# Optimization experiments

Measured on AMD Instinct MI355X. Metric: run time of the kernel, lower is better.

The kernel has to match this reference:

```python
import jax, jax.numpy as jnp
import numpy as np

U = 128  # GRU units
NIDS = 1000  # shared-state table rows

def hard_sigmoid(x):
    return jnp.clip(0.2 * x + 0.5, 0.0, 1.0)

def setup_inputs() -> dict:
    key = jax.random.key(0)
    ks = jax.random.split(key, 8)
    B, T, F = 4096, 200, 18
    inputs = jax.random.normal(ks[0], (B, T, F), dtype=jnp.float32)
    ids = jax.random.randint(ks[1], (B, T), 0, NIDS)
    inputs = inputs.at[:, :, 0].set(ids.astype(jnp.float32))
    kernel = jax.random.normal(ks[2], (F, 3 * U), dtype=jnp.float32) * 0.15
    recurrent_kernel = jax.random.normal(ks[3], (U, 3 * U), dtype=jnp.float32) * 0.08
    bias = jnp.zeros((3 * U,), dtype=jnp.float32)
    shared0 = jnp.zeros((NIDS, U), dtype=jnp.float32)
    w1 = jax.random.normal(ks[4], (U, 64), dtype=jnp.float32) * 0.1
    b1 = jnp.zeros((64,), dtype=jnp.float32)
    w2 = jax.random.normal(ks[5], (64, 1), dtype=jnp.float32) * 0.1
    b2 = jnp.zeros((1,), dtype=jnp.float32)
    return {"inputs": inputs, "kernel": kernel, "recurrent_kernel": recurrent_kernel,
            "bias": bias, "shared0": shared0, "w1": w1, "b1": b1, "w2": w2, "b2": b2}

def reference(inputs, kernel, recurrent_kernel, bias, shared0, w1, b1, w2, b2):
    # inputs: [B, T, F]; column 0 holds card ids (float-encoded).
    def step(carry, x_t):
        shared = carry  # [NIDS, U]
        ids = x_t[:, 0].astype(jnp.int32)          # [B]
        h = shared[ids]                             # gather [B, U]
        mx = x_t @ kernel + bias                    # [B, 3U]
        mh = h @ recurrent_kernel[:, :2 * U]        # [B, 2U]
        z = hard_sigmoid(mx[:, :U] + mh[:, :U])
        r = hard_sigmoid(mx[:, U:2 * U] + mh[:, U:])
        hh = jnp.tanh(mx[:, 2 * U:] + (r * h) @ recurrent_kernel[:, 2 * U:])
        h_new = z * h + (1.0 - z) * hh
        shared = shared.at[ids].set(h_new)          # scatter update
        return shared, h_new
    xs = jnp.swapaxes(inputs, 0, 1)                 # [T, B, F]
    _, hs = jax.lax.scan(step, shared0, xs)
    h_last = hs[-1]                                 # RNN returns last output [B, U]
    # dropout is identity at inference
    d = jax.nn.relu(h_last @ w1 + b1)
    out = jax.nn.sigmoid(d @ w2 + b2)               # [B, 1]
    return out
```

## Files before the change

kernel.cpp:

```cpp
#include <hip/hip_runtime.h>
#include <math.h>

#define Bz   4096
#define Tz   200
#define Fz   18
#define Uz   128
#define NIDS 1000
#define NCH  4
#define NWG  250

__device__ __forceinline__ float hsig(float x) {
    return fminf(fmaxf(fmaf(x, 0.2f, 0.5f), 0.0f), 1.0f);
}
__device__ __forceinline__ float rlane(float v, int l) {
    return __int_as_float(__builtin_amdgcn_readlane(__float_as_int(v), l));
}

__global__ void k_winner(const float* __restrict__ in, int* __restrict__ win) {
    int idx = blockIdx.x * blockDim.x + threadIdx.x;
    if (idx >= Bz * Tz) return;
    int b = idx / Tz, t = idx - b * Tz;
    int id = (int)in[(size_t)idx * Fz];
    id = min(max(id, 0), NIDS - 1);
    atomicMax(&win[t * NIDS + id], b);
}

template<bool MASK>
__device__ __forceinline__ void gstep(
    int tid, int w, int lane, int l15,
    const float (&wzr)[16][4], const float (&wh)[16][2],
    const float (&wk1)[3][4], const float (&wk2)[3][2],
    int f0, int f1, int f2,
    float breg, float breg2,
    float4* hlds, float4* ubuf, float4* zbuf, float4* p1, float4* p2,
    float xa, float xb, int4 act)
{
    float4 hd4 = hlds[w * 16 + l15];
    float hdj[4] = {hd4.x, hd4.y, hd4.z, hd4.w};
    float az[4][4];
#pragma unroll
    for (int i = 0; i < 4; ++i) { az[i][0]=0.f; az[i][1]=0.f; az[i][2]=0.f; az[i][3]=0.f; }

    int fs[3] = {f0, f1, f2};
#pragma unroll
    for (int ff = 0; ff < 3; ++ff) {
        int fb = fs[ff];
#pragma unroll
        for (int j = 0; j < 4; ++j) {
            float xv = (j < 2) ? rlane(xa, j * 18 + fb) : rlane(xb, (j - 2) * 18 + fb);
#pragma unroll
            for (int i = 0; i < 4; ++i) az[i][j] = fmaf(xv, wk1[ff][i], az[i][j]);
        }
    }
#pragma unroll
    for (int kl = 0; kl < 16; ++kl) {
#pragma unroll
        for (int j = 0; j < 4; ++j) {
            float hv = rlane(hdj[j], kl);
#pragma unroll
            for (int i = 0; i < 4; ++i) az[i][j] = fmaf(hv, wzr[kl][i], az[i][j]);
        }
    }
#pragma unroll
    for (int i = 0; i < 4; ++i)
        p1[w * 256 + lane + 64 * i] = make_float4(az[i][0], az[i][1], az[i][2], az[i][3]);
    __syncthreads();

    if (tid < 256) {
        int c = tid;
        float4 s = p1[c];
#pragma unroll
        for (int ww = 1; ww < 8; ++ww) {
            float4 q = p1[ww * 256 + c];
            s.x += q.x; s.y += q.y; s.z += q.z; s.w += q.w;
        }
        s.x += breg; s.y += breg; s.z += breg; s.w += breg;
        if (c < 128) {
            zbuf[c] = make_float4(hsig(s.x), hsig(s.y), hsig(s.z), hsig(s.w));
        } else {
            int cc = c - 128;
            float4 ho = hlds[cc];
            ubuf[cc] = make_float4(hsig(s.x) * ho.x, hsig(s.y) * ho.y,
                                   hsig(s.z) * ho.z, hsig(s.w) * ho.w);
        }
    }
    __syncthreads();

    float4 ud4 = ubuf[w * 16 + l15];
    float udj[4] = {ud4.x, ud4.y, ud4.z, ud4.w};
    float p[2][4];
#pragma unroll
    for (int i = 0; i < 2; ++i) { p[i][0]=0.f; p[i][1]=0.f; p[i][2]=0.f; p[i][3]=0.f; }
#pragma unroll
    for (int ff = 0; ff < 3; ++ff) {
        int fb = fs[ff];
#pragma unroll
        for (int j = 0; j < 4; ++j) {
            float xv = (j < 2) ? rlane(xa, j * 18 + fb) : rlane(xb, (j - 2) * 18 + fb);
#pragma unroll
            for (int i = 0; i < 2; ++i) p[i][j] = fmaf(xv, wk2[ff][i], p[i][j]);
        }
    }
#pragma unroll
    for (int kl = 0; kl < 16; ++kl) {
#pragma unroll
        for (int j = 0; j < 4; ++j) {
            float uv = rlane(udj[j], kl);
#pragma unroll
            for (int i = 0; i < 2; ++i) p[i][j] = fmaf(uv, wh[kl][i], p[i][j]);
        }
    }
    p2[w * 128 + lane]      = make_float4(p[0][0], p[0][1], p[0][2], p[0][3]);
    p2[w * 128 + lane + 64] = make_float4(p[1][0], p[1][1], p[1][2], p[1][3]);
    __syncthreads();

    if (tid < 128) {
        int c = tid;
        float4 s = p2[c];
#pragma unroll
        for (int ww = 1; ww < 8; ++ww) {
            float4 q = p2[ww * 128 + c];
            s.x += q.x; s.y += q.y; s.z += q.z; s.w += q.w;
        }
        float hh0 = tanhf(s.x + breg2), hh1 = tanhf(s.y + breg2);
        float hh2 = tanhf(s.z + breg2), hh3 = tanhf(s.w + breg2);
        float4 z = zbuf[c], ho = hlds[c];
        float n0 = fmaf(z.x, ho.x - hh0, hh0);
        float n1 = fmaf(z.y, ho.y - hh1, hh1);
        float n2 = fmaf(z.z, ho.z - hh2, hh2);
        float n3 = fmaf(z.w, ho.w - hh3, hh3);
        if (MASK) {
            if (act.x < 0) n0 = ho.x;
            if (act.y < 0) n1 = ho.y;
            if (act.z < 0) n2 = ho.z;
            if (act.w < 0) n3 = ho.w;
        }
        hlds[c] = make_float4(n0, n1, n2, n3);
    }
    __syncthreads();
}

#define LOAD_WEIGHTS                                                         \
    float wzr[16][4], wh[16][2], wk1[3][4], wk2[3][2];                       \
    _Pragma("unroll")                                                        \
    for (int kl = 0; kl < 16; ++kl) {                                        \
        int row = (w * 16 + kl) * 384;                                       \
        _Pragma("unroll")                                                    \
        for (int i = 0; i < 4; ++i) wzr[kl][i] = rk[row + lane + 64 * i];    \
        _Pragma("unroll")                                                    \
        for (int i = 0; i < 2; ++i) wh[kl][i] = rk[row + 256 + lane + 64*i]; \
    }                                                                        \
    int f0 = 2 * w, f1 = 2 * w + 1, f2 = (w < 2) ? 16 + w : 0;               \
    {                                                                        \
        int r0 = f0 * 384, r1 = f1 * 384, r2 = f2 * 384;                     \
        _Pragma("unroll")                                                    \
        for (int i = 0; i < 4; ++i) {                                        \
            wk1[0][i] = ker[r0 + lane + 64 * i];                             \
            wk1[1][i] = ker[r1 + lane + 64 * i];                             \
            wk1[2][i] = (w < 2) ? ker[r2 + lane + 64 * i] : 0.0f;            \
        }                                                                    \
        _Pragma("unroll")                                                    \
        for (int i = 0; i < 2; ++i) {                                        \
            wk2[0][i] = ker[r0 + 256 + lane + 64 * i];                       \
            wk2[1][i] = ker[r1 + 256 + lane + 64 * i];                       \
            wk2[2][i] = (w < 2) ? ker[r2 + 256 + lane + 64 * i] : 0.0f;      \
        }                                                                    \
    }                                                                        \
    float breg  = (tid < 256) ? bias[tid] : 0.0f;                            \
    float breg2 = (tid < 128) ? bias[256 + tid] : 0.0f;

__global__ __launch_bounds__(512, 2)
void k_scan(const float* __restrict__ in,  const float* __restrict__ ker,
            const float* __restrict__ rk,  const float* __restrict__ bias,
            const float* __restrict__ sh0, const int* __restrict__ win,
            float* __restrict__ sfinal)
{
    const int tid  = threadIdx.x;
    const int bx   = blockIdx.x;
    const int w    = tid >> 6;
    const int lane = tid & 63;
    const int l15  = lane & 15;

    __shared__ __align__(16) float4 hlds[Uz], ubuf[Uz], zbuf[Uz];
    __shared__ __align__(16) float4 p1[8 * 256];
    __shared__ __align__(16) float4 p2[8 * 128];

    LOAD_WEIGHTS

    ((float*)hlds)[tid] = sh0[(bx * 4 + (tid & 3)) * Uz + (tid >> 2)];

    const int4* winp = (const int4*)win;
    int4 wv_cur = winp[bx];
    int4 wv_nxt = winp[NWG + bx];

    auto ldx = [&](int4 wv, int t, int jb) -> float {
        if (lane >= 36) return 0.0f;
        int j = lane / 18, f = lane - j * 18;
        int jj = jb + j;
        int b = (jj == 0) ? wv.x : (jj == 1) ? wv.y : (jj == 2) ? wv.z : wv.w;
        if (b < 0) return 0.0f;
        return in[((size_t)b * Tz + t) * Fz + f];
    };
    float xa = ldx(wv_cur, 0, 0), xb = ldx(wv_cur, 0, 2);
    __syncthreads();

    for (int t = 0; t < Tz - 1; ++t) {
        int tf = (t + 2 < Tz) ? t + 2 : Tz - 1;
        int4  wv_fut = winp[tf * NWG + bx];
        float xaN = ldx(wv_nxt, t + 1, 0);
        float xbN = ldx(wv_nxt, t + 1, 2);

        gstep<true>(tid, w, lane, l15, wzr, wh, wk1, wk2, f0, f1, f2,
                    breg, breg2, hlds, ubuf, zbuf, p1, p2, xa, xb, wv_cur);

        xa = xaN; xb = xbN; wv_cur = wv_nxt; wv_nxt = wv_fut;
    }

    sfinal[bx * 512 + tid] = ((float*)hlds)[tid];
}

__global__ __launch_bounds__(512, 2)
void k_final(const float* __restrict__ in,  const float* __restrict__ ker,
             const float* __restrict__ rk,  const float* __restrict__ bias,
             const float* __restrict__ sfinal,
             const float* __restrict__ w1,  const float* __restrict__ b1,
             const float* __restrict__ w2,  const float* __restrict__ b2,
             float* __restrict__ out)
{
    const int tid  = threadIdx.x;
    const int w    = tid >> 6;
    const int lane = tid & 63;
    const int l15  = lane & 15;

    __shared__ __align__(16) float4 hlds[Uz], ubuf[Uz], zbuf[Uz];
    __shared__ __align__(16) float4 p1[8 * 256];
    __shared__ __align__(16) float4 p2[8 * 128];

    LOAD_WEIGHTS

    for (int it = 0; it < 4; ++it) {
        int bbase = blockIdx.x * 16 + it * 4;
        {
            int j  = tid & 3, c = tid >> 2;
            int id = (int)in[((size_t)(bbase + j) * Tz + (Tz - 1)) * Fz];
            id = min(max(id, 0), NIDS - 1);
            ((float*)hlds)[tid] = sfinal[((id >> 2) * Uz + c) * 4 + (id & 3)];
        }
        float xa = 0.0f, xb = 0.0f;
        if (lane < 36) {
            int j = lane / 18, f = lane - j * 18;
            xa = in[((size_t)(bbase + j)     * Tz + (Tz - 1)) * Fz + f];
            xb = in[((size_t)(bbase + 2 + j) * Tz + (Tz - 1)) * Fz + f];
        }
        __syncthreads();

        gstep<false>(tid, w, lane, l15, wzr, wh, wk1, wk2, f0, f1, f2,
                     breg, breg2, hlds, ubuf, zbuf, p1, p2, xa, xb,
                     make_int4(0, 0, 0, 0));

        if (tid < 256) {
            int j  = tid >> 6, un = tid & 63;
            float dacc = b1[un];
#pragma unroll
            for (int k = 0; k < Uz; ++k)
                dacc = fmaf(((const float*)hlds)[k * 4 + j], w1[k * 64 + un], dacc);
            float v = fmaxf(dacc, 0.0f) * w2[un];
#pragma unroll
            for (int off = 32; off > 0; off >>= 1) v += __shfl_xor(v, off, 64);
            if (un == 0)
                out[bbase + j] = 1.0f / (1.0f + expf(-(v + b2[0])));
        }
        __syncthreads();
    }
}

extern "C" void kernel_launch(void* const* d_in, const int* in_sizes, int n_in,
                              void* d_out, int out_size, void* d_ws, size_t ws_size,
                              hipStream_t stream) {
    const float* in   = (const float*)d_in[0];
    const float* ker  = (const float*)d_in[1];
    const float* rk   = (const float*)d_in[2];
    const float* bias = (const float*)d_in[3];
    const float* sh0  = (const float*)d_in[4];
    const float* w1   = (const float*)d_in[5];
    const float* b1   = (const float*)d_in[6];
    const float* w2   = (const float*)d_in[7];
    const float* b2   = (const float*)d_in[8];
    float* out = (float*)d_out;

    int*   win    = (int*)d_ws;
    float* sfinal = (float*)((char*)d_ws + (size_t)Tz * NIDS * sizeof(int));

    hipMemsetAsync(win, 0xFF, (size_t)Tz * NIDS * sizeof(int), stream);

    hipLaunchKernelGGL(k_winner, dim3((Bz * Tz + 255) / 256), dim3(256), 0, stream,
                       in, win);
    hipLaunchKernelGGL(k_scan, dim3(NWG), dim3(512), 0, stream,
                       in, ker, rk, bias, sh0, win, sfinal);
    hipLaunchKernelGGL(k_final, dim3(Bz / 16), dim3(512), 0, stream,
                       in, ker, rk, bias, sfinal, w1, b1, w2, b2, out);
}
```

Measured before the change: 1.206 ms.

## Split GRU step work across 1024 threads per workgroup to shorten per-step latency

```diff
diff --git a/kernel.cpp b/kernel.cpp
--- a/kernel.cpp
+++ b/kernel.cpp
@@ -27,167 +27,172 @@
 
 template<bool MASK>
 __device__ __forceinline__ void gstep(
-    int tid, int w, int lane, int l15,
-    const float (&wzr)[16][4], const float (&wh)[16][2],
-    const float (&wk1)[3][4], const float (&wk2)[3][2],
-    int f0, int f1, int f2,
-    float breg, float breg2,
-    float4* hlds, float4* ubuf, float4* zbuf, float4* p1, float4* p2,
+    int tid, int w, int p, int hw, int lane, int l15, int l7,
+    const float (&wzr)[16][2], const float (&wh)[8][2],
+    const float (&wk1)[3][2], const float (&wk2)[2][2],
+    int f0, int f1, int f2, int g0, int g1,
+    float breg1, float breg2,
+    float* hldsf, float* ubuff, float* zbuff, float4* pbuf, float* pbuff,
     float xa, float xb, int4 act)
 {
-    float4 hd4 = hlds[w * 16 + l15];
+    float4 hd4 = ((const float4*)hldsf)[p * 16 + l15];
     float hdj[4] = {hd4.x, hd4.y, hd4.z, hd4.w};
-    float az[4][4];
-#pragma unroll
-    for (int i = 0; i < 4; ++i) { az[i][0]=0.f; az[i][1]=0.f; az[i][2]=0.f; az[i][3]=0.f; }
-
-    int fs[3] = {f0, f1, f2};
-#pragma unroll
-    for (int ff = 0; ff < 3; ++ff) {
-        int fb = fs[ff];
-#pragma unroll
-        for (int j = 0; j < 4; ++j) {
-            float xv = (j < 2) ? rlane(xa, j * 18 + fb) : rlane(xb, (j - 2) * 18 + fb);
-#pragma unroll
-            for (int i = 0; i < 4; ++i) az[i][j] = fmaf(xv, wk1[ff][i], az[i][j]);
-        }
+    float az[2][4];
+#pragma unroll
+    for (int j = 0; j < 4; ++j) { az[0][j] = 0.f; az[1][j] = 0.f; }
+
+#pragma unroll
+    for (int j = 0; j < 4; ++j) {
+        float src = (j < 2) ? xa : xb;
+        int base = (j & 1) * 18;
+        float xv0 = rlane(src, base + f0);
+        float xv1 = rlane(src, base + f1);
+        float xv2 = rlane(src, base + f2);
+        az[0][j] = fmaf(xv0, wk1[0][0], az[0][j]);
+        az[1][j] = fmaf(xv0, wk1[0][1], az[1][j]);
+        az[0][j] = fmaf(xv1, wk1[1][0], az[0][j]);
+        az[1][j] = fmaf(xv1, wk1[1][1], az[1][j]);
+        az[0][j] = fmaf(xv2, wk1[2][0], az[0][j]);
+        az[1][j] = fmaf(xv2, wk1[2][1], az[1][j]);
     }
 #pragma unroll
     for (int kl = 0; kl < 16; ++kl) {
 #pragma unroll
         for (int j = 0; j < 4; ++j) {
             float hv = rlane(hdj[j], kl);
-#pragma unroll
-            for (int i = 0; i < 4; ++i) az[i][j] = fmaf(hv, wzr[kl][i], az[i][j]);
-        }
-    }
-#pragma unroll
-    for (int i = 0; i < 4; ++i)
-        p1[w * 256 + lane + 64 * i] = make_float4(az[i][0], az[i][1], az[i][2], az[i][3]);
-    __syncthreads();
-
-    if (tid < 256) {
-        int c = tid;
-        float4 s = p1[c];
-#pragma unroll
-        for (int ww = 1; ww < 8; ++ww) {
-            float4 q = p1[ww * 256 + c];
-            s.x += q.x; s.y += q.y; s.z += q.z; s.w += q.w;
-        }
-        s.x += breg; s.y += breg; s.z += breg; s.w += breg;
-        if (c < 128) {
-            zbuf[c] = make_float4(hsig(s.x), hsig(s.y), hsig(s.z), hsig(s.w));
+            az[0][j] = fmaf(hv, wzr[kl][0], az[0][j]);
+            az[1][j] = fmaf(hv, wzr[kl][1], az[1][j]);
+        }
+    }
+    pbuf[p * 256 + hw * 128 + lane]      = make_float4(az[0][0], az[0][1], az[0][2], az[0][3]);
+    pbuf[p * 256 + hw * 128 + lane + 64] = make_float4(az[1][0], az[1][1], az[1][2], az[1][3]);
+    __syncthreads();
+
+    {
+        float s = breg1;
+#pragma unroll
+        for (int pp = 0; pp < 8; ++pp) s += pbuff[pp * 1024 + tid];
+        if (tid < 512) {
+            zbuff[tid] = hsig(s);
         } else {
-            int cc = c - 128;
-            float4 ho = hlds[cc];
-            ubuf[cc] = make_float4(hsig(s.x) * ho.x, hsig(s.y) * ho.y,
-                                   hsig(s.z) * ho.z, hsig(s.w) * ho.w);
-        }
-    }
-    __syncthreads();
-
-    float4 ud4 = ubuf[w * 16 + l15];
+            int cu = tid - 512;
+            ubuff[cu] = hsig(s) * hldsf[cu];
+        }
+    }
+    __syncthreads();
+
+    float4 ud4 = ((const float4*)ubuff)[w * 8 + l7];
     float udj[4] = {ud4.x, ud4.y, ud4.z, ud4.w};
-    float p[2][4];
-#pragma unroll
-    for (int i = 0; i < 2; ++i) { p[i][0]=0.f; p[i][1]=0.f; p[i][2]=0.f; p[i][3]=0.f; }
-#pragma unroll
-    for (int ff = 0; ff < 3; ++ff) {
-        int fb = fs[ff];
-#pragma unroll
-        for (int j = 0; j < 4; ++j) {
-            float xv = (j < 2) ? rlane(xa, j * 18 + fb) : rlane(xb, (j - 2) * 18 + fb);
-#pragma unroll
-            for (int i = 0; i < 2; ++i) p[i][j] = fmaf(xv, wk2[ff][i], p[i][j]);
-        }
-    }
-#pragma unroll
-    for (int kl = 0; kl < 16; ++kl) {
+    float pa[2][4];
+#pragma unroll
+    for (int j = 0; j < 4; ++j) { pa[0][j] = 0.f; pa[1][j] = 0.f; }
+#pragma unroll
+    for (int j = 0; j < 4; ++j) {
+        float src = (j < 2) ? xa : xb;
+        int base = (j & 1) * 18;
+        float xv0 = rlane(src, base + g0);
+        float xv1 = rlane(src, base + g1);
+        pa[0][j] = fmaf(xv0, wk2[0][0], pa[0][j]);
+        pa[1][j] = fmaf(xv0, wk2[0][1], pa[1][j]);
+        pa[0][j] = fmaf(xv1, wk2[1][0], pa[0][j]);
+        pa[1][j] = fmaf(xv1, wk2[1][1], pa[1][j]);
+    }
+#pragma unroll
+    for (int kl = 0; kl < 8; ++kl) {
 #pragma unroll
         for (int j = 0; j < 4; ++j) {
             float uv = rlane(udj[j], kl);
-#pragma unroll
-            for (int i = 0; i < 2; ++i) p[i][j] = fmaf(uv, wh[kl][i], p[i][j]);
-        }
-    }
-    p2[w * 128 + lane]      = make_float4(p[0][0], p[0][1], p[0][2], p[0][3]);
-    p2[w * 128 + lane + 64] = make_float4(p[1][0], p[1][1], p[1][2], p[1][3]);
-    __syncthreads();
-
-    if (tid < 128) {
-        int c = tid;
-        float4 s = p2[c];
-#pragma unroll
-        for (int ww = 1; ww < 8; ++ww) {
-            float4 q = p2[ww * 128 + c];
-            s.x += q.x; s.y += q.y; s.z += q.z; s.w += q.w;
-        }
-        float hh0 = tanhf(s.x + breg2), hh1 = tanhf(s.y + breg2);
-        float hh2 = tanhf(s.z + breg2), hh3 = tanhf(s.w + breg2);
-        float4 z = zbuf[c], ho = hlds[c];
-        float n0 = fmaf(z.x, ho.x - hh0, hh0);
-        float n1 = fmaf(z.y, ho.y - hh1, hh1);
-        float n2 = fmaf(z.z, ho.z - hh2, hh2);
-        float n3 = fmaf(z.w, ho.w - hh3, hh3);
+            pa[0][j] = fmaf(uv, wh[kl][0], pa[0][j]);
+            pa[1][j] = fmaf(uv, wh[kl][1], pa[1][j]);
+        }
+    }
+    pbuf[w * 128 + lane]      = make_float4(pa[0][0], pa[0][1], pa[0][2], pa[0][3]);
+    pbuf[w * 128 + lane + 64] = make_float4(pa[1][0], pa[1][1], pa[1][2], pa[1][3]);
+    __syncthreads();
+
+    if (tid < 512) {
+        float s = breg2;
+#pragma unroll
+        for (int ww = 0; ww < 16; ++ww) s += pbuff[ww * 512 + tid];
+        float hh = tanhf(s);
+        float z  = zbuff[tid];
+        float ho = hldsf[tid];
+        float hn = fmaf(z, ho - hh, hh);
         if (MASK) {
-            if (act.x < 0) n0 = ho.x;
-            if (act.y < 0) n1 = ho.y;
-            if (act.z < 0) n2 = ho.z;
-            if (act.w < 0) n3 = ho.w;
-        }
-        hlds[c] = make_float4(n0, n1, n2, n3);
-    }
-    __syncthreads();
-}
-
-#define LOAD_WEIGHTS                                                         \
-    float wzr[16][4], wh[16][2], wk1[3][4], wk2[3][2];                       \
-    _Pragma("unroll")                                                        \
-    for (int kl = 0; kl < 16; ++kl) {                                        \
-        int row = (w * 16 + kl) * 384;                                       \
-        _Pragma("unroll")                                                    \
-        for (int i = 0; i < 4; ++i) wzr[kl][i] = rk[row + lane + 64 * i];    \
-        _Pragma("unroll")                                                    \
-        for (int i = 0; i < 2; ++i) wh[kl][i] = rk[row + 256 + lane + 64*i]; \
-    }                                                                        \
-    int f0 = 2 * w, f1 = 2 * w + 1, f2 = (w < 2) ? 16 + w : 0;               \
-    {                                                                        \
-        int r0 = f0 * 384, r1 = f1 * 384, r2 = f2 * 384;                     \
-        _Pragma("unroll")                                                    \
-        for (int i = 0; i < 4; ++i) {                                        \
-            wk1[0][i] = ker[r0 + lane + 64 * i];                             \
-            wk1[1][i] = ker[r1 + lane + 64 * i];                             \
-            wk1[2][i] = (w < 2) ? ker[r2 + lane + 64 * i] : 0.0f;            \
-        }                                                                    \
-        _Pragma("unroll")                                                    \
-        for (int i = 0; i < 2; ++i) {                                        \
-            wk2[0][i] = ker[r0 + 256 + lane + 64 * i];                       \
-            wk2[1][i] = ker[r1 + 256 + lane + 64 * i];                       \
-            wk2[2][i] = (w < 2) ? ker[r2 + 256 + lane + 64 * i] : 0.0f;      \
-        }                                                                    \
-    }                                                                        \
-    float breg  = (tid < 256) ? bias[tid] : 0.0f;                            \
-    float breg2 = (tid < 128) ? bias[256 + tid] : 0.0f;
-
-__global__ __launch_bounds__(512, 2)
+            int j = tid & 3;
+            int av = (j == 0) ? act.x : (j == 1) ? act.y : (j == 2) ? act.z : act.w;
+            if (av < 0) hn = ho;
+        }
+        hldsf[tid] = hn;
+    }
+    __syncthreads();
+}
+
+#define LOAD_WEIGHTS                                                          \
+    float wzr[16][2], wh[8][2], wk1[3][2], wk2[2][2];                         \
+    _Pragma("unroll")                                                         \
+    for (int kl = 0; kl < 16; ++kl) {                                         \
+        int row = (p * 16 + kl) * 384 + hw * 128 + lane;                      \
+        wzr[kl][0] = rk[row];                                                 \
+        wzr[kl][1] = rk[row + 64];                                            \
+    }                                                                         \
+    _Pragma("unroll")                                                         \
+    for (int kl = 0; kl < 8; ++kl) {                                          \
+        int row = (w * 8 + kl) * 384 + 256 + lane;                            \
+        wh[kl][0] = rk[row];                                                  \
+        wh[kl][1] = rk[row + 64];                                             \
+    }                                                                         \
+    int f0 = 2 * p, f1 = 2 * p + 1, f2 = (p < 2) ? 16 + p : 0;                \
+    {                                                                         \
+        int r0 = f0 * 384 + hw * 128 + lane;                                  \
+        int r1 = f1 * 384 + hw * 128 + lane;                                  \
+        int r2 = f2 * 384 + hw * 128 + lane;                                  \
+        wk1[0][0] = ker[r0];  wk1[0][1] = ker[r0 + 64];                       \
+        wk1[1][0] = ker[r1];  wk1[1][1] = ker[r1 + 64];                       \
+        wk1[2][0] = (p < 2) ? ker[r2] : 0.0f;                                 \
+        wk1[2][1] = (p < 2) ? ker[r2 + 64] : 0.0f;                            \
+    }                                                                         \
+    int g0 = w, g1 = (w < 2) ? 16 + w : 0;                                    \
+    {                                                                         \
+        int r0 = g0 * 384 + 256 + lane;                                       \
+        int r1 = g1 * 384 + 256 + lane;                                       \
+        wk2[0][0] = ker[r0];  wk2[0][1] = ker[r0 + 64];                       \
+        wk2[1][0] = (w < 2) ? ker[r1] : 0.0f;                                 \
+        wk2[1][1] = (w < 2) ? ker[r1 + 64] : 0.0f;                            \
+    }                                                                         \
+    float breg1 = bias[tid >> 2];                                             \
+    float breg2 = (tid < 512) ? bias[256 + (tid >> 2)] : 0.0f;
+
+#define DECLARE_IDX                                                           \
+    const int tid  = threadIdx.x;                                             \
+    const int w    = tid >> 6;                                                \
+    const int lane = tid & 63;                                                \
+    const int p    = w >> 1;                                                  \
+    const int hw   = w & 1;                                                   \
+    const int l15  = lane & 15;                                               \
+    const int l7   = lane & 7;
+
+#define DECLARE_LDS                                                           \
+    __shared__ __align__(16) float4 hlds4[Uz], ubuf4[Uz], zbuf4[Uz];          \
+    __shared__ __align__(16) float4 pbuf[2048];    \
+    float* hldsf = (float*)hlds4;                                             \
+    float* ubuff = (float*)ubuf4;                                             \
+    float* zbuff = (float*)zbuf4;                                             \
+    float* pbuff = (float*)pbuf;
+
+__global__ __launch_bounds__(1024, 4)
 void k_scan(const float* __restrict__ in,  const float* __restrict__ ker,
             const float* __restrict__ rk,  const float* __restrict__ bias,
             const float* __restrict__ sh0, const int* __restrict__ win,
             float* __restrict__ sfinal)
 {
-    const int tid  = threadIdx.x;
-    const int bx   = blockIdx.x;
-    const int w    = tid >> 6;
-    const int lane = tid & 63;
-    const int l15  = lane & 15;
-
-    __shared__ __align__(16) float4 hlds[Uz], ubuf[Uz], zbuf[Uz];
-    __shared__ __align__(16) float4 p1[8 * 256];
-    __shared__ __align__(16) float4 p2[8 * 128];
-
+    DECLARE_IDX
+    const int bx = blockIdx.x;
+    DECLARE_LDS
     LOAD_WEIGHTS
 
-    ((float*)hlds)[tid] = sh0[(bx * 4 + (tid & 3)) * Uz + (tid >> 2)];
+    if (tid < 512)
+        hldsf[tid] = sh0[(bx * 4 + (tid & 3)) * Uz + (tid >> 2)];
 
     const int4* winp = (const int4*)win;
     int4 wv_cur = winp[bx];
@@ -210,16 +215,17 @@
         float xaN = ldx(wv_nxt, t + 1, 0);
         float xbN = ldx(wv_nxt, t + 1, 2);
 
-        gstep<true>(tid, w, lane, l15, wzr, wh, wk1, wk2, f0, f1, f2,
-                    breg, breg2, hlds, ubuf, zbuf, p1, p2, xa, xb, wv_cur);
+        gstep<true>(tid, w, p, hw, lane, l15, l7, wzr, wh, wk1, wk2,
+                    f0, f1, f2, g0, g1, breg1, breg2,
+                    hldsf, ubuff, zbuff, pbuf, pbuff, xa, xb, wv_cur);
 
         xa = xaN; xb = xbN; wv_cur = wv_nxt; wv_nxt = wv_fut;
     }
 
-    sfinal[bx * 512 + tid] = ((float*)hlds)[tid];
-}
-
-__global__ __launch_bounds__(512, 2)
+    if (tid < 512) sfinal[bx * 512 + tid] = hldsf[tid];
+}
+
+__global__ __launch_bounds__(1024, 4)
 void k_final(const float* __restrict__ in,  const float* __restrict__ ker,
              const float* __restrict__ rk,  const float* __restrict__ bias,
              const float* __restrict__ sfinal,
@@ -227,24 +233,18 @@
              const float* __restrict__ w2,  const float* __restrict__ b2,
              float* __restrict__ out)
 {
-    const int tid  = threadIdx.x;
-    const int w    = tid >> 6;
-    const int lane = tid & 63;
-    const int l15  = lane & 15;
-
-    __shared__ __align__(16) float4 hlds[Uz], ubuf[Uz], zbuf[Uz];
-    __shared__ __align__(16) float4 p1[8 * 256];
-    __shared__ __align__(16) float4 p2[8 * 128];
-
+    DECLARE_IDX
+    DECLARE_LDS
     LOAD_WEIGHTS
 
     for (int it = 0; it < 4; ++it) {
         int bbase = blockIdx.x * 16 + it * 4;
-        {
+
+        if (tid < 512) {
             int j  = tid & 3, c = tid >> 2;
             int id = (int)in[((size_t)(bbase + j) * Tz + (Tz - 1)) * Fz];
             id = min(max(id, 0), NIDS - 1);
-            ((float*)hlds)[tid] = sfinal[((id >> 2) * Uz + c) * 4 + (id & 3)];
+            hldsf[tid] = sfinal[((id >> 2) * Uz + c) * 4 + (id & 3)];
         }
         float xa = 0.0f, xb = 0.0f;
         if (lane < 36) {
@@ -254,8 +254,9 @@
         }
         __syncthreads();
 
-        gstep<false>(tid, w, lane, l15, wzr, wh, wk1, wk2, f0, f1, f2,
-                     breg, breg2, hlds, ubuf, zbuf, p1, p2, xa, xb,
+        gstep<false>(tid, w, p, hw, lane, l15, l7, wzr, wh, wk1, wk2,
+                     f0, f1, f2, g0, g1, breg1, breg2,
+                     hldsf, ubuff, zbuff, pbuf, pbuff, xa, xb,
                      make_int4(0, 0, 0, 0));
 
         if (tid < 256) {
@@ -263,7 +264,7 @@
             float dacc = b1[un];
 #pragma unroll
             for (int k = 0; k < Uz; ++k)
-                dacc = fmaf(((const float*)hlds)[k * 4 + j], w1[k * 64 + un], dacc);
+                dacc = fmaf(hldsf[k * 4 + j], w1[k * 64 + un], dacc);
             float v = fmaxf(dacc, 0.0f) * w2[un];
 #pragma unroll
             for (int off = 32; off > 0; off >>= 1) v += __shfl_xor(v, off, 64);
@@ -295,8 +296,8 @@
 
     hipLaunchKernelGGL(k_winner, dim3((Bz * Tz + 255) / 256), dim3(256), 0, stream,
                        in, win);
-    hipLaunchKernelGGL(k_scan, dim3(NWG), dim3(512), 0, stream,
+    hipLaunchKernelGGL(k_scan, dim3(NWG), dim3(1024), 0, stream,
                        in, ker, rk, bias, sh0, win, sfinal);
-    hipLaunchKernelGGL(k_final, dim3(Bz / 16), dim3(512), 0, stream,
+    hipLaunchKernelGGL(k_final, dim3(Bz / 16), dim3(1024), 0, stream,
                        in, ker, rk, bias, sfinal, w1, b1, w2, b2, out);
 }
```

Result: slower. 2.126 ms (+76.3%).
